# Optimization experiments

Measured on AMD Instinct MI355X. Metric: run time of the kernel, lower is better.

Reference implementation:

```python
import jax, jax.numpy as jnp
import numpy as np

GAMMA = 2.6
SIG0, SIG1 = 0.17, 4.86
EXP_S, EXP_F = 2.0, 0.6

F1_NP = np.array([[0.0025, 0.0125, 0.02, 0.0125, 0.0025],
                  [0.0125, 0.0625, 0.1, 0.0625, 0.0125],
                  [0.02, 0.1, 0.16, 0.1, 0.02],
                  [0.0125, 0.0625, 0.1, 0.0625, 0.0125],
                  [0.0025, 0.0125, 0.02, 0.0125, 0.0025]], dtype=np.float32)[None, None]
FILT0_NP = np.array([[0.04, 0.04, 0.05, 0.04, 0.04],
                     [0.04, 0.03, 0.04, 0.03, 0.04],
                     [0.05, 0.04, 0.05, 0.04, 0.05],
                     [0.04, 0.03, 0.04, 0.03, 0.04],
                     [0.04, 0.04, 0.05, 0.04, 0.04]], dtype=np.float32)[None, None]
FILT1_NP = np.zeros((5, 5), dtype=np.float32)
FILT1_NP[2, 2] = 1.0
FILT1_NP = FILT1_NP[None, None]


def _pad_rep(x, p):
    return jnp.pad(x, ((0, 0), (0, 0), (p, p), (p, p)), mode='edge')


def _conv(x, f, pad=0):
    return jax.lax.conv_general_dilated(
        x, f, window_strides=(1, 1), padding=[(pad, pad), (pad, pad)],
        dimension_numbers=('NCHW', 'OIHW', 'NCHW'))


def _down(img, f):
    # replicate-pad by 2, valid 5x5 conv (output same HxW), stride-2 subsample
    o = _conv(_pad_rep(img, 2), f)
    return o[:, :, ::2, ::2]


def _up(img, odd, f):
    x = _pad_rep(img, 1)
    B, C, Hp, Wp = x.shape
    h, w = 2 * Hp, 2 * Wp
    o = jnp.zeros((B, C, h, w), x.dtype).at[:, :, ::2, ::2].set(4.0 * x)
    o = _conv(o, f, pad=2)
    return o[:, :, 2:h - 2 - odd[0], 2:w - 2 - odd[1]]


def _laplacian_pyramid(img, n_lev, f):
    pyr = []
    o = img
    for _ in range(n_lev - 1):
        g = _down(o, f)
        odd = [g.shape[2] * 2 - o.shape[2], g.shape[3] * 2 - o.shape[3]]
        pyr.append(o - _up(g, odd, f))
        o = g
    pyr.append(o)
    return pyr


def _nlp(img, n_lev, F1, filt0, filt1):
    img = img ** (1.0 / GAMMA)
    pyr = _laplacian_pyramid(img, n_lev, F1)
    npyr = []
    for i in range(n_lev - 1):
        den = _conv(_pad_rep(jnp.abs(pyr[i]), 2), filt0) + SIG0
        npyr.append(pyr[i] / den)
    den = _conv(_pad_rep(jnp.abs(pyr[-1]), 2), filt1) + SIG1
    npyr.append(pyr[-1] / den)
    return npyr


def setup_inputs() -> dict:
    key = jax.random.key(0)
    k1, k2 = jax.random.split(key)
    B, H, W = 16, 512, 512
    h_img = jax.random.uniform(k1, (B, 1, H, W), dtype=jnp.float32)
    l_img = jax.random.uniform(k2, (B, 1, H, W), dtype=jnp.float32)
    return {
        'h_img': h_img,
        'l_img': l_img,
        'F1': jnp.asarray(F1_NP),
        'filt0': jnp.asarray(FILT0_NP),
        'filt1': jnp.asarray(FILT1_NP),
        'n_lev': 7,
    }


def reference(h_img, l_img, F1, filt0, filt1, n_lev):
    h_pyr = _nlp(h_img, n_lev, F1, filt0, filt1)
    l_pyr = _nlp(l_img, n_lev, F1, filt0, filt1)
    dis = []
    for i in range(n_lev):
        diff = jnp.abs(h_pyr[i] - l_pyr[i]) ** EXP_S
        dis.append(jnp.mean(diff, axis=(-2, -1)) ** (EXP_F / EXP_S))  # [B, 1]
    dis = jnp.concatenate(dis, axis=-1)  # [B, n_lev]
    loss = jnp.mean(dis, axis=-1) ** (1.0 / EXP_F)
    return jnp.mean(loss)
```

## Files before the change

kernel.cpp:

```cpp
#include <hip/hip_runtime.h>

#define SIG0 0.17f
#define SIG1 4.86f

__device__ __constant__ float c_filt0[25] = {
  0.04f,0.04f,0.05f,0.04f,0.04f,
  0.04f,0.03f,0.04f,0.03f,0.04f,
  0.05f,0.04f,0.05f,0.04f,0.05f,
  0.04f,0.03f,0.04f,0.03f,0.04f,
  0.04f,0.04f,0.05f,0.04f,0.04f};
__device__ __constant__ float c_f1d[5] = {0.05f,0.25f,0.4f,0.25f,0.05f};

static __device__ __forceinline__ int iclamp(int v, int lo, int hi){
  return v < lo ? lo : (v > hi ? hi : v);
}


struct FS {
  float sg[2][36][76];
  float s1[2][20][44];
  float red[4];
};
struct DS {
  float st[36][136];
  float hs[36][64];
};
struct TS {
  float A3[2][64][66];
  float A4[2][32][34];
  float A5[2][16][18];
  float A6[2][8][10];
  float red[4];
};

__device__ __forceinline__ void down_body(const float* __restrict__ in0, float* __restrict__ out0,
                                          int PSI, int PSO, int Sout, int xo0, int yo0, char* smem){
  DS* S = (DS*)smem;
  int tid = threadIdx.x;
  for (int f=tid; f<36*34; f+=256){
    int r=f/34, c4=f%34;
    *(float4*)&S->st[r][4*c4] = *(const float4*)&in0[(size_t)(2*yo0+r)*PSI + 2*xo0 + 4*c4];
  }
  __syncthreads();
  for (int f=tid; f<36*64; f+=256){
    int r=f>>6, xo=f&63;
    const float* rp = &S->st[r][2*xo+2];
    S->hs[r][xo] = 0.05f*rp[0]+0.25f*rp[1]+0.4f*rp[2]+0.25f*rp[3]+0.05f*rp[4];
  }
  __syncthreads();
  for (int f=tid; f<16*64; f+=256){
    int yo=f>>6, xo=f&63;
    int Y=yo0+yo, X=xo0+xo;
    float v = 0.05f*S->hs[2*yo][xo]+0.25f*S->hs[2*yo+1][xo]+0.4f*S->hs[2*yo+2][xo]
            +0.25f*S->hs[2*yo+3][xo]+0.05f*S->hs[2*yo+4][xo];
    int rlo=(Y==0)?0:(Y+2), rhi=(Y==Sout-1)?(Sout+3):(Y+2);
    int clo=(X==0)?0:(X+4), chi=(X==Sout-1)?(Sout+7):(X+4);
    for (int rr=rlo; rr<=rhi; rr++)
      for (int cc=clo; cc<=chi; cc++)
        out0[(size_t)rr*PSO+cc] = v;
  }
}

__global__ __launch_bounds__(256)
void k_d1(const float* __restrict__ hin, const float* __restrict__ lin,
          float* __restrict__ g1){
  __shared__ DS S;
  int xo0 = blockIdx.x*64, yo0 = blockIdx.y*16, z = blockIdx.z;
  const float* in = (z<16)? hin + (size_t)z*262144 : lin + (size_t)(z-16)*262144;
  float* out0 = g1 + (size_t)z*68640;
  int tid = threadIdx.x;
  const float e = 0.3846153846153846f;
  for (int f=tid; f<36*34; f+=256){
    int r=f/34, c4=f%34;
    int yy = iclamp(2*yo0-2+r, 0, 511);
    int xb = 2*xo0-4+4*c4;
    const float* rp = in + (size_t)yy*512;
    float4 v;
    if (xb>=0 && xb<=508) v = *(const float4*)&rp[xb];
    else { v.x=rp[iclamp(xb,0,511)]; v.y=rp[iclamp(xb+1,0,511)];
           v.z=rp[iclamp(xb+2,0,511)]; v.w=rp[iclamp(xb+3,0,511)]; }
    v.x=__powf(v.x,e); v.y=__powf(v.y,e); v.z=__powf(v.z,e); v.w=__powf(v.w,e);
    *(float4*)&S.st[r][4*c4] = v;
  }
  __syncthreads();
  for (int f=tid; f<36*64; f+=256){
    int r=f>>6, xo=f&63;
    const float* rp = &S.st[r][2*xo+2];
    S.hs[r][xo] = 0.05f*rp[0]+0.25f*rp[1]+0.4f*rp[2]+0.25f*rp[3]+0.05f*rp[4];
  }
  __syncthreads();
  for (int f=tid; f<16*64; f+=256){
    int yo=f>>6, xo=f&63;
    int Y=yo0+yo, X=xo0+xo;
    float v = 0.05f*S.hs[2*yo][xo]+0.25f*S.hs[2*yo+1][xo]+0.4f*S.hs[2*yo+2][xo]
            +0.25f*S.hs[2*yo+3][xo]+0.05f*S.hs[2*yo+4][xo];
    int rlo=(Y==0)?0:(Y+2), rhi=(Y==255)?259:(Y+2);
    int clo=(X==0)?0:(X+4), chi=(X==255)?263:(X+4);
    for (int rr=rlo; rr<=rhi; rr++)
      for (int cc=clo; cc<=chi; cc++)
        out0[(size_t)rr*264+cc] = v;
  }
}

__device__ __forceinline__ void fused_stage_s1(FS* S, const float* __restrict__ g10,
                                               const float* __restrict__ g11,
                                               int PS1, int x0, int y0){
  int tid = threadIdx.x;
  for (int f=tid; f<2*20*10; f+=256){
    int img=f/200, rem=f%200, ro=rem/10, co=rem%10;
    const float* src = img? g11 : g10;
    *(float4*)&S->s1[img][ro][4*co] = *(const float4*)&src[(size_t)(y0/2+ro)*PS1 + x0/2 + 4*co];
  }
}

__device__ __forceinline__ void fused_stage_g(FS* S, const float* __restrict__ gk0,
                                              const float* __restrict__ gk1,
                                              int PS0, int x0, int y0){
  int tid = threadIdx.x;
  for (int f=tid; f<2*36*18; f+=256){
    int img=f/648, rem=f%648, r=rem/18, q=rem%18;
    const float* src = img? gk1 : gk0;
    *(float4*)&S->sg[img][r][4*q] = *(const float4*)&src[(size_t)(y0+r)*PS0 + x0 + 4*q];
  }
}

__device__ __forceinline__ void fused_stage_in(FS* S, const float* __restrict__ h0,
                                               const float* __restrict__ l0,
                                               int x0, int y0){
  int tid = threadIdx.x;
  const float e = 0.3846153846153846f;
  for (int f=tid; f<2*36*18; f+=256){
    int img=f/648, rem=f%648, r=rem/18, q=rem%18;
    const float* src = img? l0 : h0;
    int yy = iclamp(y0-2+r, 0, 511);
    int xb = x0-4+4*q;
    const float* rp = src + (size_t)yy*512;
    float4 v;
    if (xb>=0 && xb<=508) v = *(const float4*)&rp[xb];
    else { v.x=rp[iclamp(xb,0,511)]; v.y=rp[iclamp(xb+1,0,511)];
           v.z=rp[iclamp(xb+2,0,511)]; v.w=rp[iclamp(xb+3,0,511)]; }
    v.x=__powf(v.x,e); v.y=__powf(v.y,e); v.z=__powf(v.z,e); v.w=__powf(v.w,e);
    *(float4*)&S->sg[img][r][4*q] = v;
  }
}

__device__ __forceinline__ float4 up_row(const float* __restrict__ p){
  float2 A = *(const float2*)p;
  float2 B = *(const float2*)(p+2);
  float2 C = *(const float2*)(p+4);
  float4 t;
  t.x = 0.05f*A.y + 0.4f*B.x + 0.05f*B.y;
  t.y = 0.25f*(B.x+B.y);
  t.z = 0.05f*B.x + 0.4f*B.y + 0.05f*C.x;
  t.w = 0.25f*(B.y+C.x);
  return t;
}

__device__ __forceinline__ void fused_tail(FS* S, int Simg, int x0, int y0,
                                           float* __restrict__ accum, int lev, int b){
  int tid = threadIdx.x;
  __syncthreads();

  for (int f=tid; f<2*36*18; f+=256){
    int img=f/648, rem=f%648, r=rem/18, q=rem%18;
    int ry = ((r-2)>>1)+2;
    int cq = 2*q;
    float4 u;
    if ((r&1)==0){
      float4 a = up_row(&S->s1[img][ry-1][cq]);
      float4 m = up_row(&S->s1[img][ry  ][cq]);
      float4 c2= up_row(&S->s1[img][ry+1][cq]);
      u.x = 0.2f*a.x+1.6f*m.x+0.2f*c2.x;
      u.y = 0.2f*a.y+1.6f*m.y+0.2f*c2.y;
      u.z = 0.2f*a.z+1.6f*m.z+0.2f*c2.z;
      u.w = 0.2f*a.w+1.6f*m.w+0.2f*c2.w;
    } else {
      float4 a = up_row(&S->s1[img][ry  ][cq]);
      float4 m = up_row(&S->s1[img][ry+1][cq]);
      u.x=a.x+m.x; u.y=a.y+m.y; u.z=a.z+m.z; u.w=a.w+m.w;
    }
    float4 val = *(float4*)&S->sg[img][r][4*q];
    val.x-=u.x; val.y-=u.y; val.z-=u.z; val.w-=u.w;
    *(float4*)&S->sg[img][r][4*q] = val;
  }
  __syncthreads();

  bool top=(y0==0), bot=(y0+32==Simg), lft=(x0==0), rgt=(x0+64==Simg);
  if (top||bot||lft||rgt){
    for (int f=tid; f<2*18; f+=256){
      int img=f/18, q=f%18;
      if (top){ float4 v=*(float4*)&S->sg[img][2][4*q];
                *(float4*)&S->sg[img][0][4*q]=v; *(float4*)&S->sg[img][1][4*q]=v; }
      if (bot){ float4 v=*(float4*)&S->sg[img][33][4*q];
                *(float4*)&S->sg[img][34][4*q]=v; *(float4*)&S->sg[img][35][4*q]=v; }
    }
    __syncthreads();
    for (int f=tid; f<2*36; f+=256){
      int img=f/36, r=f%36;
      if (lft){ float v=S->sg[img][r][4];  float4 vv={v,v,v,v}; *(float4*)&S->sg[img][r][0]=vv; }
      if (rgt){ float v=S->sg[img][r][67]; float4 vv={v,v,v,v}; *(float4*)&S->sg[img][r][68]=vv; }
    }
    __syncthreads();
  }

  int tx = tid & 15, ty = tid >> 4;
  int xl = 4*tx;
  float vacc = 0.f;
  float q0o0[4], q0o1[4];
  #pragma unroll
  for (int img=0; img<2; img++){
    float d0[4]={SIG0,SIG0,SIG0,SIG0}, d1[4]={SIG0,SIG0,SIG0,SIG0};
    float n0[4], n1[4];
    #pragma unroll
    for (int i=0;i<6;i++){
      float r_[12];
      *(float4*)&r_[0] = *(const float4*)&S->sg[img][2*ty+i][xl];
      *(float4*)&r_[4] = *(const float4*)&S->sg[img][2*ty+i][xl+4];
      *(float4*)&r_[8] = *(const float4*)&S->sg[img][2*ty+i][xl+8];
      if (i==2){ n0[0]=r_[4]; n0[1]=r_[5]; n0[2]=r_[6]; n0[3]=r_[7]; }
      if (i==3){ n1[0]=r_[4]; n1[1]=r_[5]; n1[2]=r_[6]; n1[3]=r_[7]; }
      if (i<5){
        #pragma unroll
        for (int jj=0;jj<5;jj++){
          float w = c_filt0[i*5+jj];
          #pragma unroll
          for (int j=0;j<4;j++) d0[j] += w*fabsf(r_[2+j+jj]);
        }
      }
      if (i>0){
        #pragma unroll
        for (int jj=0;jj<5;jj++){
          float w = c_filt0[(i-1)*5+jj];
          #pragma unroll
          for (int j=0;j<4;j++) d1[j] += w*fabsf(r_[2+j+jj]);
        }
      }
    }
    if (img==0){
      #pragma unroll
      for (int j=0;j<4;j++){ q0o0[j]=__fdividef(n0[j],d0[j]); q0o1[j]=__fdividef(n1[j],d1[j]); }
    } else {
      #pragma unroll
      for (int j=0;j<4;j++){
        float a = q0o0[j]-__fdividef(n0[j],d0[j]); vacc += a*a;
        float b2= q0o1[j]-__fdividef(n1[j],d1[j]); vacc += b2*b2;
      }
    }
  }
  #pragma unroll
  for (int off=32; off>0; off>>=1) vacc += __shfl_down(vacc, off);
  if ((tid&63)==0) S->red[tid>>6] = vacc;
  __syncthreads();
  if (tid==0)
    atomicAdd(&accum[lev*16+b], S->red[0]+S->red[1]+S->red[2]+S->red[3]);
}

static __device__ __forceinline__ void down_lds(const float* Ain, int ldi, int Sin,
                                                float* Aout, int ldo, int Sout,
                                                int tid, int NT){
  int tot = 2*Sout*Sout;
  for (int f=tid; f<tot; f+=NT){
    int img = f/(Sout*Sout), rem = f%(Sout*Sout), y=rem/Sout, x=rem%Sout;
    const float* A = Ain + img*Sin*ldi;
    float s=0.f;
    #pragma unroll
    for (int i=0;i<5;i++){
      int yy=iclamp(2*y+i-2,0,Sin-1);
      float rs=0.f;
      #pragma unroll
      for (int j=0;j<5;j++){
        int xx=iclamp(2*x+j-2,0,Sin-1);
        rs += c_f1d[j]*A[yy*ldi+xx];
      }
      s += c_f1d[i]*rs;
    }
    Aout[img*Sout*ldo + y*ldo + x] = s;
  }
}

static __device__ __forceinline__ void lap_lds(float* Ak, int ldk, int S,
                                               const float* Ag, int ldg,
                                               int tid, int NT){
  int Sg = S>>1;
  int tot = 2*S*S;
  for (int f=tid; f<tot; f+=NT){
    int img=f/(S*S), rem=f%(S*S), y=rem/S, x=rem%S;
    const float* G = Ag + img*Sg*ldg;
    int y2=y>>1, x2=x>>1;
    int ry0,ry1,ry2; float wy0,wy1,wy2;
    if (!(y&1)){ ry0=iclamp(y2-1,0,Sg-1); ry1=y2; ry2=iclamp(y2+1,0,Sg-1); wy0=0.2f; wy1=1.6f; wy2=0.2f; }
    else { ry0=y2; ry1=iclamp(y2+1,0,Sg-1); ry2=y2; wy0=1.f; wy1=1.f; wy2=0.f; }
    int cx0,cx1,cx2; float wx0,wx1,wx2;
    if (!(x&1)){ cx0=iclamp(x2-1,0,Sg-1); cx1=x2; cx2=iclamp(x2+1,0,Sg-1); wx0=0.05f; wx1=0.4f; wx2=0.05f; }
    else { cx0=x2; cx1=iclamp(x2+1,0,Sg-1); cx2=x2; wx0=0.25f; wx1=0.25f; wx2=0.f; }
    float u0 = wx0*G[ry0*ldg+cx0]+wx1*G[ry0*ldg+cx1]+wx2*G[ry0*ldg+cx2];
    float u1 = wx0*G[ry1*ldg+cx0]+wx1*G[ry1*ldg+cx1]+wx2*G[ry1*ldg+cx2];
    float u2 = wx0*G[ry2*ldg+cx0]+wx1*G[ry2*ldg+cx1]+wx2*G[ry2*ldg+cx2];
    Ak[img*S*ldk + y*ldk + x] -= wy0*u0+wy1*u1+wy2*u2;
  }
}

static __device__ __forceinline__ float diff_lds(const float* A, int ld, int S,
                                                 int tid, int NT){
  float v=0.f;
  const float* Ah = A;
  const float* Al = A + S*ld;
  for (int f=tid; f<S*S; f+=NT){
    int y=f/S, x=f%S;
    float dh=SIG0, dl=SIG0;
    #pragma unroll
    for (int i=0;i<5;i++){
      int yy=iclamp(y+i-2,0,S-1);
      #pragma unroll
      for (int j=0;j<5;j++){
        int xx=iclamp(x+j-2,0,S-1);
        float w=c_filt0[i*5+j];
        dh += w*fabsf(Ah[yy*ld+xx]);
        dl += w*fabsf(Al[yy*ld+xx]);
      }
    }
    float d = __fdividef(Ah[y*ld+x],dh) - __fdividef(Al[y*ld+x],dl);
    v += d*d;
  }
  return v;
}

__device__ void tail_body(const float* __restrict__ g3, float* __restrict__ accum,
                          int b, char* smem){
  TS* T = (TS*)smem;
  int tid = threadIdx.x;
  const float* s0  = g3 + (size_t)b*4896 + 148;
  const float* s1p = g3 + (size_t)(b+16)*4896 + 148;
  for (int f=tid; f<2*4096; f+=256){
    int img=f>>12, rem=f&4095, r=rem>>6, c=rem&63;
    T->A3[img][r][c] = (img? s1p : s0)[(size_t)r*72+c];
  }
  __syncthreads();
  down_lds(&T->A3[0][0][0],66,64,&T->A4[0][0][0],34,32,tid,256);
  __syncthreads();
  down_lds(&T->A4[0][0][0],34,32,&T->A5[0][0][0],18,16,tid,256);
  __syncthreads();
  down_lds(&T->A5[0][0][0],18,16,&T->A6[0][0][0],10,8,tid,256);
  __syncthreads();
  lap_lds(&T->A3[0][0][0],66,64,&T->A4[0][0][0],34,tid,256);
  __syncthreads();
  float v3 = diff_lds(&T->A3[0][0][0],66,64,tid,256);
  lap_lds(&T->A4[0][0][0],34,32,&T->A5[0][0][0],18,tid,256);
  __syncthreads();
  float v4 = diff_lds(&T->A4[0][0][0],34,32,tid,256);
  lap_lds(&T->A5[0][0][0],18,16,&T->A6[0][0][0],10,tid,256);
  __syncthreads();
  float v5 = diff_lds(&T->A5[0][0][0],18,16,tid,256);
  float v6 = 0.f;
  for (int f=tid; f<64; f+=256){
    float ch = T->A6[0][f>>3][f&7];
    float cl = T->A6[1][f>>3][f&7];
    float d = __fdividef(ch, fabsf(ch)+SIG1) - __fdividef(cl, fabsf(cl)+SIG1);
    v6 += d*d;
  }
  float vs[4] = {v3, v4, v5, v6};
  #pragma unroll
  for (int k=0;k<4;k++){
    float v = vs[k];
    #pragma unroll
    for (int off=32; off>0; off>>=1) v += __shfl_down(v, off);
    if ((tid&63)==0) T->red[tid>>6] = v;
    __syncthreads();
    if (tid==0){
      accum[(3+k)*16 + b] = T->red[0]+T->red[1]+T->red[2]+T->red[3];
    }
    __syncthreads();
  }
}

__global__ __launch_bounds__(256)
void k_d2(const float* __restrict__ h, const float* __restrict__ l,
          const float* __restrict__ g1, float* __restrict__ g2,
          float* __restrict__ accum){
  extern __shared__ char smem[];
  if (blockIdx.z < 16){
    FS* S = (FS*)smem;
    int b = blockIdx.z, x0 = blockIdx.x*64, y0 = blockIdx.y*32;
    fused_stage_in(S, h+(size_t)b*262144, l+(size_t)b*262144, x0, y0);
    fused_stage_s1(S, g1+(size_t)b*68640, g1+(size_t)(b+16)*68640, 264, x0, y0);
    fused_tail(S, 512, x0, y0, accum, 0, b);
  } else {
    int id = (blockIdx.z-16)*128 + blockIdx.y*8 + blockIdx.x;
    int db = id>>4, dby = (id>>1)&7, dbx = id&1;
    down_body(g1+(size_t)db*68640, g2+(size_t)db*17952, 264, 136, 128, dbx*64, dby*16, smem);
  }
}

__global__ __launch_bounds__(256)
void k_d4(const float* __restrict__ g1, float* __restrict__ g2,
          float* __restrict__ g3, float* __restrict__ accum){
  extern __shared__ char smem[];
  if (blockIdx.z < 16){
    FS* S = (FS*)smem;
    int b = blockIdx.z, x0 = blockIdx.x*64, y0 = blockIdx.y*32;
    fused_stage_g(S, g1+(size_t)b*68640, g1+(size_t)(b+16)*68640, 264, x0, y0);
    fused_stage_s1(S, g2+(size_t)b*17952, g2+(size_t)(b+16)*17952, 136, x0, y0);
    fused_tail(S, 256, x0, y0, accum, 1, b);
  } else {
    int id = (blockIdx.z-16)*32 + blockIdx.y*4 + blockIdx.x;
    int db = id>>2, dby = id&3;
    down_body(g2+(size_t)db*17952, g3+(size_t)db*4896, 136, 72, 64, 0, dby*16, smem);
  }
}

__global__ __launch_bounds__(256)
void k_d5(const float* __restrict__ g2, const float* __restrict__ g3,
          float* __restrict__ accum){
  extern __shared__ char smem[];
  if (blockIdx.z < 16){
    FS* S = (FS*)smem;
    int b = blockIdx.z, x0 = blockIdx.x*64, y0 = blockIdx.y*32;
    fused_stage_g(S, g2+(size_t)b*17952, g2+(size_t)(b+16)*17952, 136, x0, y0);
    fused_stage_s1(S, g3+(size_t)b*4896, g3+(size_t)(b+16)*4896, 72, x0, y0);
    fused_tail(S, 128, x0, y0, accum, 2, b);
  } else {
    int id = (blockIdx.z-16)*8 + blockIdx.y*2 + blockIdx.x;
    tail_body(g3, accum, id, smem);
  }
}

__global__ __launch_bounds__(64)
void k_d6(const float* __restrict__ accum, float* __restrict__ out){
  __shared__ float s[16];
  int b = threadIdx.x;
  if (b < 16){
    float m = 0.f;
    #pragma unroll
    for (int k=0;k<7;k++){
      int hw = (512>>k)*(512>>k);
      float mean = accum[k*16+b] / (float)hw;
      m += powf(mean, 0.3f);
    }
    m *= (1.0f/7.0f);
    s[b] = powf(m, 1.6666666666666667f);
  }
  __syncthreads();
  if (b == 0){
    float t = 0.f;
    #pragma unroll
    for (int i=0;i<16;i++) t += s[i];
    out[0] = t * (1.0f/16.0f);
  }
}

extern "C" void kernel_launch(void* const* d_in, const int* in_sizes, int n_in,
                              void* d_out, int out_size, void* d_ws, size_t ws_size,
                              hipStream_t stream){
  const float* h = (const float*)d_in[0];
  const float* l = (const float*)d_in[1];
  float* out = (float*)d_out;
  float* ws = (float*)d_ws;

  float* g1 = ws;
  float* g2 = g1 + 2196480;
  float* g3 = g2 + 574464;
  float* accum = g3 + 156672;

  hipMemsetAsync(accum, 0, 112*sizeof(float), stream);

  k_d1<<<dim3(4,16,32), 256, 0, stream>>>(h, l, g1);
  k_d2<<<dim3(8,16,20), 256, sizeof(FS), stream>>>(h, l, g1, g2, accum);
  k_d4<<<dim3(4,8,20),  256, sizeof(FS), stream>>>(g1, g2, g3, accum);
  k_d5<<<dim3(2,4,18),  256, sizeof(TS), stream>>>(g2, g3, accum);
  k_d6<<<1, 64, 0, stream>>>(accum, out);
}
```

Baseline: 174.3 us.

## Factor filt0 convolution into box sums and split images across thread halves

The fused tail's 5x5 normalization filter is rewritten algebraically. The filter equals 0.04 times a box sum, plus a 0.01 correction on the 0.05 taps, minus 0.01 on the 0.03 taps. Horizontal and vertical box sums are built with running add/subtract, which removes most per-tap multiply-adds. Work is also redistributed so each half of the block handles one image over a 4x4 output patch, exchanging normalized values through a new shared buffer with an extra barrier. Index decomposition in the staging loops replaces divides by 648 and 200 with comparisons. The running-sum form can change floating-point rounding slightly, uses more registers, and leaves half the threads idle during the final reduction.

```diff
diff --git a/kernel.cpp b/kernel.cpp
--- a/kernel.cpp
+++ b/kernel.cpp
@@ -19,6 +19,7 @@
 struct FS {
   float sg[2][36][76];
   float s1[2][20][44];
+  float qbuf[128*20];
   float red[4];
 };
 struct DS {
@@ -106,8 +107,9 @@
                                                const float* __restrict__ g11,
                                                int PS1, int x0, int y0){
   int tid = threadIdx.x;
-  for (int f=tid; f<2*20*10; f+=256){
-    int img=f/200, rem=f%200, ro=rem/10, co=rem%10;
+  for (int f=tid; f<400; f+=256){
+    int img = f>=200; int fi = img ? f-200 : f;
+    int ro = fi/10, co = fi - 10*ro;
     const float* src = img? g11 : g10;
     *(float4*)&S->s1[img][ro][4*co] = *(const float4*)&src[(size_t)(y0/2+ro)*PS1 + x0/2 + 4*co];
   }
@@ -117,8 +119,9 @@
                                               const float* __restrict__ gk1,
                                               int PS0, int x0, int y0){
   int tid = threadIdx.x;
-  for (int f=tid; f<2*36*18; f+=256){
-    int img=f/648, rem=f%648, r=rem/18, q=rem%18;
+  for (int f=tid; f<1296; f+=256){
+    int img = f>=648; int fi = img ? f-648 : f;
+    int r = fi/18, q = fi - 18*r;
     const float* src = img? gk1 : gk0;
     *(float4*)&S->sg[img][r][4*q] = *(const float4*)&src[(size_t)(y0+r)*PS0 + x0 + 4*q];
   }
@@ -129,8 +132,9 @@
                                                int x0, int y0){
   int tid = threadIdx.x;
   const float e = 0.3846153846153846f;
-  for (int f=tid; f<2*36*18; f+=256){
-    int img=f/648, rem=f%648, r=rem/18, q=rem%18;
+  for (int f=tid; f<1296; f+=256){
+    int img = f>=648; int fi = img ? f-648 : f;
+    int r = fi/18, q = fi - 18*r;
     const float* src = img? l0 : h0;
     int yy = iclamp(y0-2+r, 0, 511);
     int xb = x0-4+4*q;
@@ -161,8 +165,9 @@
   int tid = threadIdx.x;
   __syncthreads();
 
-  for (int f=tid; f<2*36*18; f+=256){
-    int img=f/648, rem=f%648, r=rem/18, q=rem%18;
+  for (int f=tid; f<1296; f+=256){
+    int img = f>=648; int fi = img ? f-648 : f;
+    int r = fi/18, q = fi - 18*r;
     int ry = ((r-2)>>1)+2;
     int cq = 2*q;
     float4 u;
@@ -203,48 +208,60 @@
     __syncthreads();
   }
 
-  int tx = tid & 15, ty = tid >> 4;
-  int xl = 4*tx;
+  int t = tid & 127;
+  int img = tid >> 7;
+  int qx = t & 15, qy = t >> 4;
+  int r0 = 4*qy;
+  int c0 = 4*qx + 2;
+
+  float a[8][8];
+  #pragma unroll
+  for (int r=0;r<8;r++){
+    const float* rp = &S->sg[img][r0+r][c0];
+    *(float2*)&a[r][0] = *(const float2*)&rp[0];
+    *(float4*)&a[r][2] = *(const float4*)&rp[2];
+    *(float2*)&a[r][6] = *(const float2*)&rp[6];
+  }
+
+  float h[8][4];
+  #pragma unroll
+  for (int r=0;r<8;r++){
+    float s = ((fabsf(a[r][0])+fabsf(a[r][1])) + (fabsf(a[r][2])+fabsf(a[r][3]))) + fabsf(a[r][4]);
+    h[r][0] = s;
+    h[r][1] = h[r][0] - fabsf(a[r][0]) + fabsf(a[r][5]);
+    h[r][2] = h[r][1] - fabsf(a[r][1]) + fabsf(a[r][6]);
+    h[r][3] = h[r][2] - fabsf(a[r][2]) + fabsf(a[r][7]);
+  }
+
+  float q[4][4];
+  #pragma unroll
+  for (int c=0;c<4;c++){
+    float T = (h[0][c]+h[1][c]) + (h[2][c]+h[3][c]) + h[4][c];
+    #pragma unroll
+    for (int k=0;k<4;k++){
+      if (k) T += h[k+4][c] - h[k-1][c];
+      float s05 = (fabsf(a[k][c+2]) + fabsf(a[k+2][c])) + (fabsf(a[k+2][c+2])
+                + fabsf(a[k+2][c+4])) + fabsf(a[k+4][c+2]);
+      float s03 = (fabsf(a[k+1][c+1]) + fabsf(a[k+1][c+3]))
+                + (fabsf(a[k+3][c+1]) + fabsf(a[k+3][c+3]));
+      float den = SIG0 + 0.04f*T + 0.01f*s05 - 0.01f*s03;
+      q[k][c] = __fdividef(a[k+2][c+2], den);
+    }
+  }
+
+  if (img==1){
+    #pragma unroll
+    for (int k=0;k<4;k++)
+      *(float4*)&S->qbuf[t*20 + 4*k] = make_float4(q[k][0],q[k][1],q[k][2],q[k][3]);
+  }
+  __syncthreads();
   float vacc = 0.f;
-  float q0o0[4], q0o1[4];
-  #pragma unroll
-  for (int img=0; img<2; img++){
-    float d0[4]={SIG0,SIG0,SIG0,SIG0}, d1[4]={SIG0,SIG0,SIG0,SIG0};
-    float n0[4], n1[4];
-    #pragma unroll
-    for (int i=0;i<6;i++){
-      float r_[12];
-      *(float4*)&r_[0] = *(const float4*)&S->sg[img][2*ty+i][xl];
-      *(float4*)&r_[4] = *(const float4*)&S->sg[img][2*ty+i][xl+4];
-      *(float4*)&r_[8] = *(const float4*)&S->sg[img][2*ty+i][xl+8];
-      if (i==2){ n0[0]=r_[4]; n0[1]=r_[5]; n0[2]=r_[6]; n0[3]=r_[7]; }
-      if (i==3){ n1[0]=r_[4]; n1[1]=r_[5]; n1[2]=r_[6]; n1[3]=r_[7]; }
-      if (i<5){
-        #pragma unroll
-        for (int jj=0;jj<5;jj++){
-          float w = c_filt0[i*5+jj];
-          #pragma unroll
-          for (int j=0;j<4;j++) d0[j] += w*fabsf(r_[2+j+jj]);
-        }
-      }
-      if (i>0){
-        #pragma unroll
-        for (int jj=0;jj<5;jj++){
-          float w = c_filt0[(i-1)*5+jj];
-          #pragma unroll
-          for (int j=0;j<4;j++) d1[j] += w*fabsf(r_[2+j+jj]);
-        }
-      }
-    }
-    if (img==0){
-      #pragma unroll
-      for (int j=0;j<4;j++){ q0o0[j]=__fdividef(n0[j],d0[j]); q0o1[j]=__fdividef(n1[j],d1[j]); }
-    } else {
-      #pragma unroll
-      for (int j=0;j<4;j++){
-        float a = q0o0[j]-__fdividef(n0[j],d0[j]); vacc += a*a;
-        float b2= q0o1[j]-__fdividef(n1[j],d1[j]); vacc += b2*b2;
-      }
+  if (img==0){
+    #pragma unroll
+    for (int k=0;k<4;k++){
+      float4 o = *(const float4*)&S->qbuf[t*20 + 4*k];
+      float d0=q[k][0]-o.x, d1=q[k][1]-o.y, d2=q[k][2]-o.z, d3=q[k][3]-o.w;
+      vacc += (d0*d0+d1*d1)+(d2*d2+d3*d3);
     }
   }
   #pragma unroll
```

Measured after the change: 172.8 us. No clear change (-0.8%).

## Halve row tiles, restructure fused Laplacian stage with per-thread strips and separable filt0

Applied to the files above, without the earlier changes.

Tile height is halved in all stages (16-row fused tiles, 8-row downsample tiles), which doubles the grid and shrinks shared memory so more blocks can run per CU. The fused stage is rewritten so each thread loads 12-wide strips and computes the upsample for a 12-wide row segment. The filt0 divisive normalization is evaluated through sliding-window box sums plus a small correction term, and the h/l comparison pairs adjacent lanes via a shuffle. The extra halo rows per tile add redundant loads, and the algebraic rewrite of filt0 may slightly change floating-point rounding.

```diff
diff --git a/kernel.cpp b/kernel.cpp
--- a/kernel.cpp
+++ b/kernel.cpp
@@ -17,13 +17,13 @@
 
 
 struct FS {
-  float sg[2][36][76];
-  float s1[2][20][44];
+  float sg[2][20][76];
+  float s1[2][12][44];
   float red[4];
 };
 struct DS {
-  float st[36][136];
-  float hs[36][64];
+  float st[20][136];
+  float hs[20][64];
 };
 struct TS {
   float A3[2][64][66];
@@ -37,18 +37,18 @@
                                           int PSI, int PSO, int Sout, int xo0, int yo0, char* smem){
   DS* S = (DS*)smem;
   int tid = threadIdx.x;
-  for (int f=tid; f<36*34; f+=256){
-    int r=f/34, c4=f%34;
+  for (int f=tid; f<20*34; f+=256){
+    int r=f/34, c4=f-34*r;
     *(float4*)&S->st[r][4*c4] = *(const float4*)&in0[(size_t)(2*yo0+r)*PSI + 2*xo0 + 4*c4];
   }
   __syncthreads();
-  for (int f=tid; f<36*64; f+=256){
+  for (int f=tid; f<20*64; f+=256){
     int r=f>>6, xo=f&63;
     const float* rp = &S->st[r][2*xo+2];
     S->hs[r][xo] = 0.05f*rp[0]+0.25f*rp[1]+0.4f*rp[2]+0.25f*rp[3]+0.05f*rp[4];
   }
   __syncthreads();
-  for (int f=tid; f<16*64; f+=256){
+  for (int f=tid; f<8*64; f+=256){
     int yo=f>>6, xo=f&63;
     int Y=yo0+yo, X=xo0+xo;
     float v = 0.05f*S->hs[2*yo][xo]+0.25f*S->hs[2*yo+1][xo]+0.4f*S->hs[2*yo+2][xo]
@@ -65,13 +65,13 @@
 void k_d1(const float* __restrict__ hin, const float* __restrict__ lin,
           float* __restrict__ g1){
   __shared__ DS S;
-  int xo0 = blockIdx.x*64, yo0 = blockIdx.y*16, z = blockIdx.z;
+  int xo0 = blockIdx.x*64, yo0 = blockIdx.y*8, z = blockIdx.z;
   const float* in = (z<16)? hin + (size_t)z*262144 : lin + (size_t)(z-16)*262144;
   float* out0 = g1 + (size_t)z*68640;
   int tid = threadIdx.x;
   const float e = 0.3846153846153846f;
-  for (int f=tid; f<36*34; f+=256){
-    int r=f/34, c4=f%34;
+  for (int f=tid; f<20*34; f+=256){
+    int r=f/34, c4=f-34*r;
     int yy = iclamp(2*yo0-2+r, 0, 511);
     int xb = 2*xo0-4+4*c4;
     const float* rp = in + (size_t)yy*512;
@@ -83,13 +83,13 @@
     *(float4*)&S.st[r][4*c4] = v;
   }
   __syncthreads();
-  for (int f=tid; f<36*64; f+=256){
+  for (int f=tid; f<20*64; f+=256){
     int r=f>>6, xo=f&63;
     const float* rp = &S.st[r][2*xo+2];
     S.hs[r][xo] = 0.05f*rp[0]+0.25f*rp[1]+0.4f*rp[2]+0.25f*rp[3]+0.05f*rp[4];
   }
   __syncthreads();
-  for (int f=tid; f<16*64; f+=256){
+  for (int f=tid; f<8*64; f+=256){
     int yo=f>>6, xo=f&63;
     int Y=yo0+yo, X=xo0+xo;
     float v = 0.05f*S.hs[2*yo][xo]+0.25f*S.hs[2*yo+1][xo]+0.4f*S.hs[2*yo+2][xo]
@@ -102,156 +102,188 @@
   }
 }
 
-__device__ __forceinline__ void fused_stage_s1(FS* S, const float* __restrict__ g10,
-                                               const float* __restrict__ g11,
-                                               int PS1, int x0, int y0){
-  int tid = threadIdx.x;
-  for (int f=tid; f<2*20*10; f+=256){
-    int img=f/200, rem=f%200, ro=rem/10, co=rem%10;
-    const float* src = img? g11 : g10;
-    *(float4*)&S->s1[img][ro][4*co] = *(const float4*)&src[(size_t)(y0/2+ro)*PS1 + x0/2 + 4*co];
-  }
-}
-
-__device__ __forceinline__ void fused_stage_g(FS* S, const float* __restrict__ gk0,
-                                              const float* __restrict__ gk1,
-                                              int PS0, int x0, int y0){
-  int tid = threadIdx.x;
-  for (int f=tid; f<2*36*18; f+=256){
-    int img=f/648, rem=f%648, r=rem/18, q=rem%18;
-    const float* src = img? gk1 : gk0;
-    *(float4*)&S->sg[img][r][4*q] = *(const float4*)&src[(size_t)(y0+r)*PS0 + x0 + 4*q];
-  }
-}
-
-__device__ __forceinline__ void fused_stage_in(FS* S, const float* __restrict__ h0,
-                                               const float* __restrict__ l0,
-                                               int x0, int y0){
-  int tid = threadIdx.x;
+template<int GAMMA>
+__device__ __forceinline__ void fused_body(FS* S,
+    const float* __restrict__ a0, const float* __restrict__ a1, int PS0,
+    const float* __restrict__ s10, const float* __restrict__ s11, int PS1,
+    int Simg, int x0, int y0, int lev, int b, float* __restrict__ accum){
+  int t = threadIdx.x;
   const float e = 0.3846153846153846f;
-  for (int f=tid; f<2*36*18; f+=256){
-    int img=f/648, rem=f%648, r=rem/18, q=rem%18;
-    const float* src = img? l0 : h0;
-    int yy = iclamp(y0-2+r, 0, 511);
-    int xb = x0-4+4*q;
-    const float* rp = src + (size_t)yy*512;
-    float4 v;
-    if (xb>=0 && xb<=508) v = *(const float4*)&rp[xb];
-    else { v.x=rp[iclamp(xb,0,511)]; v.y=rp[iclamp(xb+1,0,511)];
-           v.z=rp[iclamp(xb+2,0,511)]; v.w=rp[iclamp(xb+3,0,511)]; }
-    v.x=__powf(v.x,e); v.y=__powf(v.y,e); v.z=__powf(v.z,e); v.w=__powf(v.w,e);
-    *(float4*)&S->sg[img][r][4*q] = v;
-  }
-}
-
-__device__ __forceinline__ float4 up_row(const float* __restrict__ p){
-  float2 A = *(const float2*)p;
-  float2 B = *(const float2*)(p+2);
-  float2 C = *(const float2*)(p+4);
-  float4 t;
-  t.x = 0.05f*A.y + 0.4f*B.x + 0.05f*B.y;
-  t.y = 0.25f*(B.x+B.y);
-  t.z = 0.05f*B.x + 0.4f*B.y + 0.05f*C.x;
-  t.w = 0.25f*(B.y+C.x);
-  return t;
-}
-
-__device__ __forceinline__ void fused_tail(FS* S, int Simg, int x0, int y0,
-                                           float* __restrict__ accum, int lev, int b){
-  int tid = threadIdx.x;
-  __syncthreads();
-
-  for (int f=tid; f<2*36*18; f+=256){
-    int img=f/648, rem=f%648, r=rem/18, q=rem%18;
-    int ry = ((r-2)>>1)+2;
-    int cq = 2*q;
-    float4 u;
-    if ((r&1)==0){
-      float4 a = up_row(&S->s1[img][ry-1][cq]);
-      float4 m = up_row(&S->s1[img][ry  ][cq]);
-      float4 c2= up_row(&S->s1[img][ry+1][cq]);
-      u.x = 0.2f*a.x+1.6f*m.x+0.2f*c2.x;
-      u.y = 0.2f*a.y+1.6f*m.y+0.2f*c2.y;
-      u.z = 0.2f*a.z+1.6f*m.z+0.2f*c2.z;
-      u.w = 0.2f*a.w+1.6f*m.w+0.2f*c2.w;
+
+  if (t < 240){
+    int img = t >= 120; int t2 = img ? t-120 : t;
+    int r = t2/6, q3 = t2 - 6*r;
+    float w[12];
+    if (GAMMA){
+      int yy = iclamp(y0-2+r, 0, 511);
+      int xb = x0-4+12*q3;
+      const float* rp = (img ? a1 : a0) + (size_t)yy*512;
+      if (xb >= 0 && xb <= 500){
+        *(float4*)&w[0] = *(const float4*)&rp[xb];
+        *(float4*)&w[4] = *(const float4*)&rp[xb+4];
+        *(float4*)&w[8] = *(const float4*)&rp[xb+8];
+      } else {
+        #pragma unroll
+        for (int j=0;j<12;j++) w[j] = rp[iclamp(xb+j,0,511)];
+      }
+      #pragma unroll
+      for (int j=0;j<12;j++) w[j] = __powf(w[j], e);
     } else {
-      float4 a = up_row(&S->s1[img][ry  ][cq]);
-      float4 m = up_row(&S->s1[img][ry+1][cq]);
-      u.x=a.x+m.x; u.y=a.y+m.y; u.z=a.z+m.z; u.w=a.w+m.w;
-    }
-    float4 val = *(float4*)&S->sg[img][r][4*q];
-    val.x-=u.x; val.y-=u.y; val.z-=u.z; val.w-=u.w;
-    *(float4*)&S->sg[img][r][4*q] = val;
-  }
-  __syncthreads();
-
-  bool top=(y0==0), bot=(y0+32==Simg), lft=(x0==0), rgt=(x0+64==Simg);
-  if (top||bot||lft||rgt){
-    for (int f=tid; f<2*18; f+=256){
-      int img=f/18, q=f%18;
+      const float* rp = (img ? a1 : a0) + (size_t)(y0+r)*PS0 + x0 + 12*q3;
+      *(float4*)&w[0] = *(const float4*)&rp[0];
+      *(float4*)&w[4] = *(const float4*)&rp[4];
+      *(float4*)&w[8] = *(const float4*)&rp[8];
+    }
+    float* dp = &S->sg[img][r][12*q3];
+    *(float4*)&dp[0] = *(float4*)&w[0];
+    *(float4*)&dp[4] = *(float4*)&w[4];
+    *(float4*)&dp[8] = *(float4*)&w[8];
+  }
+  if (t < 240){
+    int img = t >= 120; int t2 = img ? t-120 : t;
+    int ro = t2/10, co = t2 - 10*ro;
+    const float* src = (img ? s11 : s10) + (size_t)(y0/2+ro)*PS1 + x0/2 + 4*co;
+    *(float4*)&S->s1[img][ro][4*co] = *(const float4*)src;
+  }
+  __syncthreads();
+
+  {
+    int tt = t & 127;
+    bool ew = t < 128;
+    if (tt < 120){
+      int img = tt >= 60; int t2 = img ? tt-60 : tt;
+      int rh = t2/6, q3 = t2 - 6*rh;
+      int r = ew ? 2*rh : 2*rh+1;
+      int cb = 6*q3;
+      float B[12], C[12], u[12];
+      {
+        const float* pB = &S->s1[img][rh+1][cb];
+        const float* pC = &S->s1[img][rh+2][cb];
+        *(float4*)&B[0]=*(const float4*)&pB[0]; *(float4*)&B[4]=*(const float4*)&pB[4]; *(float4*)&B[8]=*(const float4*)&pB[8];
+        *(float4*)&C[0]=*(const float4*)&pC[0]; *(float4*)&C[4]=*(const float4*)&pC[4]; *(float4*)&C[8]=*(const float4*)&pC[8];
+      }
+      if (ew){
+        float A[12];
+        const float* pA = &S->s1[img][rh][cb];
+        *(float4*)&A[0]=*(const float4*)&pA[0]; *(float4*)&A[4]=*(const float4*)&pA[4]; *(float4*)&A[8]=*(const float4*)&pA[8];
+        #pragma unroll
+        for (int m=0;m<6;m++){
+          float hEA = 0.05f*A[m+1]+0.4f*A[m+2]+0.05f*A[m+3];
+          float hEB = 0.05f*B[m+1]+0.4f*B[m+2]+0.05f*B[m+3];
+          float hEC = 0.05f*C[m+1]+0.4f*C[m+2]+0.05f*C[m+3];
+          u[2*m]   = 0.2f*hEA + 1.6f*hEB + 0.2f*hEC;
+          float hOA = 0.25f*(A[m+2]+A[m+3]);
+          float hOB = 0.25f*(B[m+2]+B[m+3]);
+          float hOC = 0.25f*(C[m+2]+C[m+3]);
+          u[2*m+1] = 0.2f*hOA + 1.6f*hOB + 0.2f*hOC;
+        }
+      } else {
+        #pragma unroll
+        for (int m=0;m<6;m++){
+          float hEB = 0.05f*B[m+1]+0.4f*B[m+2]+0.05f*B[m+3];
+          float hEC = 0.05f*C[m+1]+0.4f*C[m+2]+0.05f*C[m+3];
+          u[2*m]   = hEB + hEC;
+          u[2*m+1] = 0.25f*(B[m+2]+B[m+3]) + 0.25f*(C[m+2]+C[m+3]);
+        }
+      }
+      float* dp = &S->sg[img][r][12*q3];
+      float v[12];
+      *(float4*)&v[0]=*(float4*)&dp[0]; *(float4*)&v[4]=*(float4*)&dp[4]; *(float4*)&v[8]=*(float4*)&dp[8];
+      #pragma unroll
+      for (int j=0;j<12;j++) v[j] -= u[j];
+      *(float4*)&dp[0]=*(float4*)&v[0]; *(float4*)&dp[4]=*(float4*)&v[4]; *(float4*)&dp[8]=*(float4*)&v[8];
+    }
+  }
+  __syncthreads();
+
+  bool top=(y0==0), bot=(y0+16==Simg), lft=(x0==0), rgt=(x0+64==Simg);
+  if (top|bot|lft|rgt){
+    for (int f=t; f<2*18; f+=256){
+      int img = f>=18; int q = img ? f-18 : f;
       if (top){ float4 v=*(float4*)&S->sg[img][2][4*q];
                 *(float4*)&S->sg[img][0][4*q]=v; *(float4*)&S->sg[img][1][4*q]=v; }
-      if (bot){ float4 v=*(float4*)&S->sg[img][33][4*q];
-                *(float4*)&S->sg[img][34][4*q]=v; *(float4*)&S->sg[img][35][4*q]=v; }
+      if (bot){ float4 v=*(float4*)&S->sg[img][17][4*q];
+                *(float4*)&S->sg[img][18][4*q]=v; *(float4*)&S->sg[img][19][4*q]=v; }
     }
     __syncthreads();
-    for (int f=tid; f<2*36; f+=256){
-      int img=f/36, r=f%36;
+    for (int f=t; f<2*20; f+=256){
+      int img = f>=20; int r = img ? f-20 : f;
       if (lft){ float v=S->sg[img][r][4];  float4 vv={v,v,v,v}; *(float4*)&S->sg[img][r][0]=vv; }
       if (rgt){ float v=S->sg[img][r][67]; float4 vv={v,v,v,v}; *(float4*)&S->sg[img][r][68]=vv; }
     }
     __syncthreads();
   }
 
-  int tx = tid & 15, ty = tid >> 4;
-  int xl = 4*tx;
   float vacc = 0.f;
-  float q0o0[4], q0o1[4];
-  #pragma unroll
-  for (int img=0; img<2; img++){
-    float d0[4]={SIG0,SIG0,SIG0,SIG0}, d1[4]={SIG0,SIG0,SIG0,SIG0};
-    float n0[4], n1[4];
-    #pragma unroll
-    for (int i=0;i<6;i++){
-      float r_[12];
-      *(float4*)&r_[0] = *(const float4*)&S->sg[img][2*ty+i][xl];
-      *(float4*)&r_[4] = *(const float4*)&S->sg[img][2*ty+i][xl+4];
-      *(float4*)&r_[8] = *(const float4*)&S->sg[img][2*ty+i][xl+8];
-      if (i==2){ n0[0]=r_[4]; n0[1]=r_[5]; n0[2]=r_[6]; n0[3]=r_[7]; }
-      if (i==3){ n1[0]=r_[4]; n1[1]=r_[5]; n1[2]=r_[6]; n1[3]=r_[7]; }
-      if (i<5){
+  {
+    int img = t & 1, quad = t >> 1;
+    int qx = quad & 15, qy = quad >> 4;
+    int cb = 4*qx, rb = 2*qy;
+    float T0[4]={0,0,0,0}, T1[4]={0,0,0,0};
+    float s5a[4], s5b[4], s3a[4], s3b[4], n0[4], n1[4];
+    #pragma unroll
+    for (int r=0;r<6;r++){
+      float w[12];
+      const float* rp = &S->sg[img][rb+r][cb];
+      *(float4*)&w[0]=*(const float4*)&rp[0];
+      *(float4*)&w[4]=*(const float4*)&rp[4];
+      *(float4*)&w[8]=*(const float4*)&rp[8];
+      float aw[8];
+      #pragma unroll
+      for (int j=0;j<8;j++) aw[j] = fabsf(w[j+2]);
+      float h0 = ((aw[0]+aw[1])+(aw[2]+aw[3]))+aw[4];
+      float h1 = h0 - aw[0] + aw[5];
+      float h2 = h1 - aw[1] + aw[6];
+      float h3 = h2 - aw[2] + aw[7];
+      float hh[4] = {h0,h1,h2,h3};
+      if (r<=4){
         #pragma unroll
-        for (int jj=0;jj<5;jj++){
-          float w = c_filt0[i*5+jj];
-          #pragma unroll
-          for (int j=0;j<4;j++) d0[j] += w*fabsf(r_[2+j+jj]);
-        }
-      }
-      if (i>0){
+        for (int c=0;c<4;c++) T0[c] += hh[c];
+      }
+      if (r>=1){
         #pragma unroll
-        for (int jj=0;jj<5;jj++){
-          float w = c_filt0[(i-1)*5+jj];
-          #pragma unroll
-          for (int j=0;j<4;j++) d1[j] += w*fabsf(r_[2+j+jj]);
-        }
-      }
-    }
-    if (img==0){
-      #pragma unroll
-      for (int j=0;j<4;j++){ q0o0[j]=__fdividef(n0[j],d0[j]); q0o1[j]=__fdividef(n1[j],d1[j]); }
-    } else {
-      #pragma unroll
-      for (int j=0;j<4;j++){
-        float a = q0o0[j]-__fdividef(n0[j],d0[j]); vacc += a*a;
-        float b2= q0o1[j]-__fdividef(n1[j],d1[j]); vacc += b2*b2;
-      }
-    }
+        for (int c=0;c<4;c++) T1[c] += hh[c];
+      }
+      if (r==0){
+        for (int c=0;c<4;c++) s5a[c] = aw[c+2];
+      }
+      if (r==1){
+        for (int c=0;c<4;c++){ s3a[c] = aw[c+1]+aw[c+3]; s5b[c] = aw[c+2]; }
+      }
+      if (r==2){
+        for (int c=0;c<4;c++){ s5a[c] += aw[c]+aw[c+2]+aw[c+4]; n0[c]=w[c+4]; s3b[c] = aw[c+1]+aw[c+3]; }
+      }
+      if (r==3){
+        for (int c=0;c<4;c++){ s3a[c] += aw[c+1]+aw[c+3]; s5b[c] += aw[c]+aw[c+2]+aw[c+4]; n1[c]=w[c+4]; }
+      }
+      if (r==4){
+        for (int c=0;c<4;c++){ s5a[c] += aw[c+2]; s3b[c] += aw[c+1]+aw[c+3]; }
+      }
+      if (r==5){
+        for (int c=0;c<4;c++) s5b[c] += aw[c+2];
+      }
+    }
+    float qv[8];
+    #pragma unroll
+    for (int c=0;c<4;c++){
+      float d0 = SIG0 + 0.04f*T0[c] + 0.01f*s5a[c] - 0.01f*s3a[c];
+      float d1 = SIG0 + 0.04f*T1[c] + 0.01f*s5b[c] - 0.01f*s3b[c];
+      qv[c]   = __fdividef(n0[c], d0);
+      qv[4+c] = __fdividef(n1[c], d1);
+    }
+    #pragma unroll
+    for (int i=0;i<8;i++){
+      float o = __shfl_xor(qv[i], 1);
+      float d = qv[i] - o;
+      vacc += d*d;
+    }
+    if (img) vacc = 0.f;
   }
   #pragma unroll
   for (int off=32; off>0; off>>=1) vacc += __shfl_down(vacc, off);
-  if ((tid&63)==0) S->red[tid>>6] = vacc;
-  __syncthreads();
-  if (tid==0)
+  if ((t&63)==0) S->red[t>>6] = vacc;
+  __syncthreads();
+  if (t==0)
     atomicAdd(&accum[lev*16+b], S->red[0]+S->red[1]+S->red[2]+S->red[3]);
 }
 
@@ -366,9 +398,8 @@
     for (int off=32; off>0; off>>=1) v += __shfl_down(v, off);
     if ((tid&63)==0) T->red[tid>>6] = v;
     __syncthreads();
-    if (tid==0){
+    if (tid==0)
       accum[(3+k)*16 + b] = T->red[0]+T->red[1]+T->red[2]+T->red[3];
-    }
     __syncthreads();
   }
 }
@@ -379,15 +410,14 @@
           float* __restrict__ accum){
   extern __shared__ char smem[];
   if (blockIdx.z < 16){
-    FS* S = (FS*)smem;
-    int b = blockIdx.z, x0 = blockIdx.x*64, y0 = blockIdx.y*32;
-    fused_stage_in(S, h+(size_t)b*262144, l+(size_t)b*262144, x0, y0);
-    fused_stage_s1(S, g1+(size_t)b*68640, g1+(size_t)(b+16)*68640, 264, x0, y0);
-    fused_tail(S, 512, x0, y0, accum, 0, b);
+    int b = blockIdx.z, x0 = blockIdx.x*64, y0 = blockIdx.y*16;
+    fused_body<1>((FS*)smem, h+(size_t)b*262144, l+(size_t)b*262144, 0,
+                  g1+(size_t)b*68640, g1+(size_t)(b+16)*68640, 264,
+                  512, x0, y0, 0, b, accum);
   } else {
-    int id = (blockIdx.z-16)*128 + blockIdx.y*8 + blockIdx.x;
-    int db = id>>4, dby = (id>>1)&7, dbx = id&1;
-    down_body(g1+(size_t)db*68640, g2+(size_t)db*17952, 264, 136, 128, dbx*64, dby*16, smem);
+    int id = (blockIdx.z-16)*256 + blockIdx.y*8 + blockIdx.x;
+    int img = id>>5, rem = id&31, xt = rem&1, yt = rem>>1;
+    down_body(g1+(size_t)img*68640, g2+(size_t)img*17952, 264, 136, 128, xt*64, yt*8, smem);
   }
 }
 
@@ -396,15 +426,14 @@
           float* __restrict__ g3, float* __restrict__ accum){
   extern __shared__ char smem[];
   if (blockIdx.z < 16){
-    FS* S = (FS*)smem;
-    int b = blockIdx.z, x0 = blockIdx.x*64, y0 = blockIdx.y*32;
-    fused_stage_g(S, g1+(size_t)b*68640, g1+(size_t)(b+16)*68640, 264, x0, y0);
-    fused_stage_s1(S, g2+(size_t)b*17952, g2+(size_t)(b+16)*17952, 136, x0, y0);
-    fused_tail(S, 256, x0, y0, accum, 1, b);
+    int b = blockIdx.z, x0 = blockIdx.x*64, y0 = blockIdx.y*16;
+    fused_body<0>((FS*)smem, g1+(size_t)b*68640, g1+(size_t)(b+16)*68640, 264,
+                  g2+(size_t)b*17952, g2+(size_t)(b+16)*17952, 136,
+                  256, x0, y0, 1, b, accum);
   } else {
-    int id = (blockIdx.z-16)*32 + blockIdx.y*4 + blockIdx.x;
-    int db = id>>2, dby = id&3;
-    down_body(g2+(size_t)db*17952, g3+(size_t)db*4896, 136, 72, 64, 0, dby*16, smem);
+    int id = (blockIdx.z-16)*64 + blockIdx.y*4 + blockIdx.x;
+    int img = id>>3, yt = id&7;
+    down_body(g2+(size_t)img*17952, g3+(size_t)img*4896, 136, 72, 64, 0, yt*8, smem);
   }
 }
 
@@ -413,13 +442,12 @@
           float* __restrict__ accum){
   extern __shared__ char smem[];
   if (blockIdx.z < 16){
-    FS* S = (FS*)smem;
-    int b = blockIdx.z, x0 = blockIdx.x*64, y0 = blockIdx.y*32;
-    fused_stage_g(S, g2+(size_t)b*17952, g2+(size_t)(b+16)*17952, 136, x0, y0);
-    fused_stage_s1(S, g3+(size_t)b*4896, g3+(size_t)(b+16)*4896, 72, x0, y0);
-    fused_tail(S, 128, x0, y0, accum, 2, b);
+    int b = blockIdx.z, x0 = blockIdx.x*64, y0 = blockIdx.y*16;
+    fused_body<0>((FS*)smem, g2+(size_t)b*17952, g2+(size_t)(b+16)*17952, 136,
+                  g3+(size_t)b*4896, g3+(size_t)(b+16)*4896, 72,
+                  128, x0, y0, 2, b, accum);
   } else {
-    int id = (blockIdx.z-16)*8 + blockIdx.y*2 + blockIdx.x;
+    int id = blockIdx.y*2 + blockIdx.x;
     tail_body(g3, accum, id, smem);
   }
 }
@@ -461,11 +489,14 @@
   float* g3 = g2 + 574464;
   float* accum = g3 + 156672;
 
-  hipMemsetAsync(accum, 0, 112*sizeof(float), stream);
-
-  k_d1<<<dim3(4,16,32), 256, 0, stream>>>(h, l, g1);
-  k_d2<<<dim3(8,16,20), 256, sizeof(FS), stream>>>(h, l, g1, g2, accum);
-  k_d4<<<dim3(4,8,20),  256, sizeof(FS), stream>>>(g1, g2, g3, accum);
-  k_d5<<<dim3(2,4,18),  256, sizeof(TS), stream>>>(g2, g3, accum);
+  (void)hipMemsetAsync(accum, 0, 112*sizeof(float), stream);
+
+  size_t fsz = sizeof(FS) > sizeof(DS) ? sizeof(FS) : sizeof(DS);
+  size_t tsz = sizeof(TS);
+
+  k_d1<<<dim3(4,32,32), 256, 0, stream>>>(h, l, g1);
+  k_d2<<<dim3(8,32,20), 256, fsz, stream>>>(h, l, g1, g2, accum);
+  k_d4<<<dim3(4,16,20), 256, fsz, stream>>>(g1, g2, g3, accum);
+  k_d5<<<dim3(2,8,17),  256, tsz, stream>>>(g2, g3, accum);
   k_d6<<<1, 64, 0, stream>>>(accum, out);
 }
```

Measured after the change: 177.7 us. No clear change (+2.0%).
